# Performance work log

Hardware: AMD Instinct MI355X
Metric: run time of the kernel (lower is better)

The kernel has to match this reference:

```python
import jax, jax.numpy as jnp
import numpy as np

N = 10000      # nodes
E = 160000     # edges (before self-loops)
F_IN = 128     # num_features
H1, D1 = 4, 256   # conv1: 4 heads x 256, concat -> 1024
D2 = 256          # conv2: 1 head x 256
NEG_SLOPE = 0.2


def setup_inputs() -> dict:
    key = jax.random.key(0)
    ks = jax.random.split(key, 12)
    def p(k, shape, fan):
        return jax.random.normal(k, shape, jnp.float32) / np.float32(np.sqrt(fan))
    return {
        "x": jax.random.normal(ks[0], (N, F_IN), jnp.float32),
        "edge_index": jax.random.randint(ks[1], (2, E), 0, N, jnp.int32),
        "W1": p(ks[2], (F_IN, H1 * D1), F_IN),
        "att_src1": p(ks[3], (H1, D1), D1),
        "att_dst1": p(ks[4], (H1, D1), D1),
        "b1": jnp.zeros((H1 * D1,), jnp.float32),
        "lin1_W": p(ks[5], (F_IN, H1 * D1), F_IN),
        "lin1_b": jnp.zeros((H1 * D1,), jnp.float32),
        "W2": p(ks[6], (H1 * D1, D2), H1 * D1),
        "att_src2": p(ks[7], (1, D2), D2),
        "att_dst2": p(ks[8], (1, D2), D2),
        "b2": jnp.zeros((D2,), jnp.float32),
        "lin2_W": p(ks[9], (H1 * D1, D2), H1 * D1),
        "lin2_b": jnp.zeros((D2,), jnp.float32),
    }


def gat_layer(x, src, dst, W, a_src, a_dst, b, heads, d):
    """PyG-style GATConv: transform, edgewise LeakyReLU attention,
    segment-softmax over destination neighborhoods, scatter-add, concat heads."""
    n = x.shape[0]
    h = (x @ W).reshape(n, heads, d)                       # [N, H, D]
    s_src = jnp.einsum('nhd,hd->nh', h, a_src)             # per-node scores
    s_dst = jnp.einsum('nhd,hd->nh', h, a_dst)
    e = jax.nn.leaky_relu(s_src[src] + s_dst[dst], NEG_SLOPE)   # [E, H]
    m = jax.ops.segment_max(e, dst, num_segments=n)        # stable softmax per dst
    p = jnp.exp(e - m[dst])
    z = jax.ops.segment_sum(p, dst, num_segments=n)
    alpha = p / (z[dst] + 1e-16)                           # [E, H]
    msg = h[src] * alpha[:, :, None]                       # [E, H, D]
    out = jax.ops.segment_sum(msg, dst, num_segments=n)    # [N, H, D]
    return out.reshape(n, heads * d) + b, alpha


def reference(x, edge_index, W1, att_src1, att_dst1, b1, lin1_W, lin1_b,
              W2, att_src2, att_dst2, b2, lin2_W, lin2_b):
    n = x.shape[0]
    loop = jnp.arange(n, dtype=edge_index.dtype)           # add self-loops (PyG default)
    src = jnp.concatenate([edge_index[0], loop])
    dst = jnp.concatenate([edge_index[1], loop])
    h1, alpha1 = gat_layer(x, src, dst, W1, att_src1, att_dst1, b1, H1, D1)
    h1 = jax.nn.elu(h1 + x @ lin1_W + lin1_b)              # conv1 + lin1 residual, ELU
    h2, _ = gat_layer(h1, src, dst, W2, att_src2, att_dst2, b2, 1, D2)
    out = h2 + h1 @ lin2_W + lin2_b                        # conv2 + lin2 residual
    return out, alpha1
```

## Files before the change

### kernel.cpp

```cpp
#include <hip/hip_runtime.h>
#include <hip/hip_bf16.h>
#include <math.h>

#define NN   10000
#define EE   160000
#define ETOT 170000
#define FIN  128
#define C1   1024
#define NH1  4
#define D1   256
#define D2   256

typedef __attribute__((ext_vector_type(8))) short bf16x8;
typedef __attribute__((ext_vector_type(4))) float f32x4;

__device__ __forceinline__ float b2f(unsigned short u)
{
    union { unsigned int i; float f; } c; c.i = (unsigned int)u << 16; return c.f;
}
__device__ __forceinline__ unsigned short f2b(float x)
{
    return __builtin_bit_cast(unsigned short, __float2bfloat16(x));
}
__device__ __forceinline__ void split1(float x, unsigned short &h, unsigned short &l)
{
    __hip_bfloat16 hb = __float2bfloat16(x);
    float r = x - __bfloat162float(hb);
    h = __builtin_bit_cast(unsigned short, hb);
    l = __builtin_bit_cast(unsigned short, __float2bfloat16(r));
}

__global__ __launch_bounds__(256)
void split_A(const float* __restrict__ X, unsigned short* __restrict__ A2, int M, int K)
{
    int idx = blockIdx.x * 256 + threadIdx.x;
    int kq4 = K >> 2;
    if (idx >= M * kq4) return;
    int m = idx / kq4, kq = idx % kq4;
    float4 v = *(const float4*)&X[(size_t)m * K + kq * 4];
    ushort4 h, l;
    split1(v.x, h.x, l.x); split1(v.y, h.y, l.y);
    split1(v.z, h.z, l.z); split1(v.w, h.w, l.w);
    unsigned short* row = A2 + (size_t)m * (2 * K);
    *(ushort4*)&row[kq * 4]     = h;
    *(ushort4*)&row[K + kq * 4] = l;
}

__global__ __launch_bounds__(256)
void split_Bt(const float* __restrict__ B0, const float* __restrict__ B1,
              int K, int N0, int Ntot, unsigned short* __restrict__ Bt)
{
    int idx = blockIdx.x * 256 + threadIdx.x;
    int total = Ntot * (K >> 2);
    if (idx >= total) return;
    int n = idx % Ntot;
    int kq = idx / Ntot;
    int k = kq * 4;
    const float* B; int nc, nb;
    if (n < N0) { B = B0; nc = n; nb = N0; }
    else        { B = B1; nc = n - N0; nb = Ntot - N0; }
    float v0 = B[(size_t)(k + 0) * nb + nc];
    float v1 = B[(size_t)(k + 1) * nb + nc];
    float v2 = B[(size_t)(k + 2) * nb + nc];
    float v3 = B[(size_t)(k + 3) * nb + nc];
    ushort4 h, l;
    split1(v0, h.x, l.x); split1(v1, h.y, l.y);
    split1(v2, h.z, l.z); split1(v3, h.w, l.w);
    unsigned short* row = Bt + (size_t)n * (3 * K);
    *(ushort4*)&row[k]         = h;
    *(ushort4*)&row[K + k]     = h;
    *(ushort4*)&row[2 * K + k] = l;
}

__device__ __forceinline__ void glds16(const void* g, void* l)
{
    __builtin_amdgcn_global_load_lds((const __attribute__((address_space(1))) void*)g,
                                     (__attribute__((address_space(3))) void*)l, 16, 0, 0);
}

template<int BN, int WM, int WN>
__global__ __launch_bounds__(256)
void gemm_split(const unsigned short* __restrict__ A, int lda, int ka2,
                const unsigned short* __restrict__ Bt, int keff,
                unsigned short* __restrict__ outPb, float* __restrict__ outR,
                int M, int nsplit, int ldR,
                const float* __restrict__ bias0, const float* __restrict__ bias1)
{
    constexpr int BM  = 128;
    constexpr int WTM = BM / WM;
    constexpr int WTN = BN / WN;
    constexpr int FJ  = WTM / 16;
    constexpr int FI  = WTN / 16;
    constexpr int NCH = (BM + BN) / 16;
    constexpr int CPW = NCH / 4;

    __shared__ __align__(16) unsigned short sA[BM * 32];
    __shared__ __align__(16) unsigned short sB[BN * 32];
    const int tid = threadIdx.x;
    const int w = tid >> 6, lane = tid & 63;
    const int m0 = blockIdx.y * BM;
    const int n0 = blockIdx.x * BN;
    const int wm = w / WN, wn = w % WN;

    f32x4 acc[FI][FJ] = {};

    const unsigned short* gp[CPW];
    unsigned short*       lp[CPW];
    bool isa[CPW];
    #pragma unroll
    for (int cc = 0; cc < CPW; ++cc) {
        int c = w * CPW + cc;
        if (c < BM / 16) {
            int gm = m0 + c * 16 + (lane >> 2);
            if (gm >= M) gm = M - 1;
            gp[cc] = A + (size_t)gm * lda + (lane & 3) * 8;
            lp[cc] = &sA[c * 512];
            isa[cc] = true;
        } else {
            int r = (c - BM / 16) * 16 + (lane >> 2);
            gp[cc] = Bt + (size_t)(n0 + r) * keff + (lane & 3) * 8;
            lp[cc] = &sB[(c - BM / 16) * 512];
            isa[cc] = false;
        }
    }

    const int rA = wm * WTM + (lane & 15);
    const int rB = wn * WTN + (lane & 15);
    const int koff = (lane >> 4) * 8;

    for (int kk = 0; kk < keff; kk += 32) {
        const int kA = (kk >= ka2) ? (kk - ka2) : kk;
        #pragma unroll
        for (int cc = 0; cc < CPW; ++cc)
            glds16(gp[cc] + (isa[cc] ? kA : kk), lp[cc]);
        __syncthreads();
        bf16x8 av[FJ], bv[FI];
        #pragma unroll
        for (int f = 0; f < FI; ++f)
            bv[f] = *(const bf16x8*)&sB[(rB + f * 16) * 32 + koff];
        #pragma unroll
        for (int f = 0; f < FJ; ++f)
            av[f] = *(const bf16x8*)&sA[(rA + f * 16) * 32 + koff];
        #pragma unroll
        for (int fj = 0; fj < FJ; ++fj)
            #pragma unroll
            for (int fi = 0; fi < FI; ++fi)
                acc[fi][fj] = __builtin_amdgcn_mfma_f32_16x16x32_bf16(
                    bv[fi], av[fj], acc[fi][fj], 0, 0, 0);
        __syncthreads();
    }

    const int lrow = lane & 15;
    const int lcol = (lane >> 4) << 2;
    #pragma unroll
    for (int fj = 0; fj < FJ; ++fj) {
        int row = m0 + wm * WTM + fj * 16 + lrow;
        if (row >= M) continue;
        #pragma unroll
        for (int fi = 0; fi < FI; ++fi) {
            int col = n0 + wn * WTN + fi * 16 + lcol;
            f32x4 v = acc[fi][fj];
            if (col < nsplit) {
                ushort4 o;
                o.x = f2b(v[0]); o.y = f2b(v[1]); o.z = f2b(v[2]); o.w = f2b(v[3]);
                *(ushort4*)&outPb[(size_t)row * nsplit + col] = o;
            } else {
                int c = col - nsplit;
                const float4 g0 = *(const float4*)&bias0[c];
                const float4 g1 = *(const float4*)&bias1[c];
                v[0] += g0.x + g1.x; v[1] += g0.y + g1.y;
                v[2] += g0.z + g1.z; v[3] += g0.w + g1.w;
                *(f32x4*)&outR[(size_t)row * ldR + c] = v;
            }
        }
    }
}

__global__ __launch_bounds__(256)
void scores_h4(const unsigned short* __restrict__ h, const float* __restrict__ a_src,
               const float* __restrict__ a_dst, float* __restrict__ s_src,
               float* __restrict__ s_dst)
{
    const int n = blockIdx.x;
    const int w = threadIdx.x >> 6;
    const int lane = threadIdx.x & 63;
    ushort4 u = *(const ushort4*)&h[(size_t)n * C1 + w * D1 + lane * 4];
    float4 as = ((const float4*)&a_src[w * D1])[lane];
    float4 ad = ((const float4*)&a_dst[w * D1])[lane];
    float vx = b2f(u.x), vy = b2f(u.y), vz = b2f(u.z), vw = b2f(u.w);
    float ss = vx * as.x + vy * as.y + vz * as.z + vw * as.w;
    float sd = vx * ad.x + vy * ad.y + vz * ad.z + vw * ad.w;
    #pragma unroll
    for (int off = 32; off; off >>= 1) {
        ss += __shfl_xor(ss, off);
        sd += __shfl_xor(sd, off);
    }
    if (lane == 0) { s_src[n * NH1 + w] = ss; s_dst[n * NH1 + w] = sd; }
}

__global__ __launch_bounds__(256)
void scores_h1(const unsigned short* __restrict__ h, const float* __restrict__ a_src,
               const float* __restrict__ a_dst, float* __restrict__ s_src,
               float* __restrict__ s_dst)
{
    const int n = blockIdx.x * 4 + (threadIdx.x >> 6);
    if (n >= NN) return;
    const int lane = threadIdx.x & 63;
    ushort4 u = *(const ushort4*)&h[(size_t)n * D2 + lane * 4];
    float4 as = ((const float4*)a_src)[lane];
    float4 ad = ((const float4*)a_dst)[lane];
    float vx = b2f(u.x), vy = b2f(u.y), vz = b2f(u.z), vw = b2f(u.w);
    float ss = vx * as.x + vy * as.y + vz * as.z + vw * as.w;
    float sd = vx * ad.x + vy * ad.y + vz * ad.z + vw * ad.w;
    #pragma unroll
    for (int off = 32; off; off >>= 1) {
        ss += __shfl_xor(ss, off);
        sd += __shfl_xor(sd, off);
    }
    if (lane == 0) { s_src[n] = ss; s_dst[n] = sd; }
}

__global__ void count_deg(const int* __restrict__ dstp, int* __restrict__ cnt)
{
    int e = blockIdx.x * 256 + threadIdx.x;
    if (e >= ETOT) return;
    int d = (e < EE) ? dstp[e] : (e - EE);
    atomicAdd(&cnt[d], 1);
}

__global__ __launch_bounds__(1024)
void scan_kernel(const int* __restrict__ cnt, int* __restrict__ row_ptr)
{
    __shared__ int part[1024];
    const int t = threadIdx.x;
    int local[10];
    int s = 0;
    #pragma unroll
    for (int j = 0; j < 10; ++j) {
        int idx = t * 10 + j;
        local[j] = s;
        s += (idx < NN) ? cnt[idx] : 0;
    }
    part[t] = s;
    __syncthreads();
    for (int off = 1; off < 1024; off <<= 1) {
        int v = (t >= off) ? part[t - off] : 0;
        __syncthreads();
        part[t] += v;
        __syncthreads();
    }
    int prefix = (t > 0) ? part[t - 1] : 0;
    #pragma unroll
    for (int j = 0; j < 10; ++j) {
        int idx = t * 10 + j;
        if (idx < NN) row_ptr[idx] = prefix + local[j];
    }
    if (t == 0) row_ptr[NN] = ETOT;
}

__global__ void scatter_edges(const int* __restrict__ srcp, const int* __restrict__ dstp,
                              const int* __restrict__ row_ptr, int* __restrict__ fill,
                              int* __restrict__ csr_src, int* __restrict__ csr_eid)
{
    int e = blockIdx.x * 256 + threadIdx.x;
    if (e >= ETOT) return;
    int s, d;
    if (e < EE) { s = srcp[e]; d = dstp[e]; } else { s = d = e - EE; }
    int pos = row_ptr[d] + atomicAdd(&fill[d], 1);
    csr_src[pos] = s;
    csr_eid[pos] = e;
}

__global__ __launch_bounds__(256)
void aggregate1(const unsigned short* __restrict__ h1b, const float* __restrict__ s_src,
                const float* __restrict__ s_dst,
                const int* __restrict__ row_ptr, const int* __restrict__ csr_src,
                const int* __restrict__ csr_eid, const float* __restrict__ base_in,
                unsigned short* __restrict__ a2stk, float* __restrict__ alpha_out)
{
    const int n = blockIdx.x;
    const int t = threadIdx.x;
    const int h = t >> 6;
    const int lane = t & 63;
    const int start = row_ptr[n], end = row_ptr[n + 1];
    const float sd = s_dst[n * NH1 + h];

    float m = -1e30f;
    for (int i = start + lane; i < end; i += 64) {
        float sc = s_src[csr_src[i] * NH1 + h] + sd;
        sc = sc > 0.f ? sc : 0.2f * sc;
        m = fmaxf(m, sc);
    }
    #pragma unroll
    for (int off = 32; off; off >>= 1) m = fmaxf(m, __shfl_xor(m, off));
    float z = 0.f;
    for (int i = start + lane; i < end; i += 64) {
        float sc = s_src[csr_src[i] * NH1 + h] + sd;
        sc = sc > 0.f ? sc : 0.2f * sc;
        z += __expf(sc - m);
    }
    #pragma unroll
    for (int off = 32; off; off >>= 1) z += __shfl_xor(z, off);
    const float invz = 1.f / (z + 1e-16f);
    for (int i = start + lane; i < end; i += 64) {
        float sc = s_src[csr_src[i] * NH1 + h] + sd;
        sc = sc > 0.f ? sc : 0.2f * sc;
        alpha_out[(size_t)csr_eid[i] * NH1 + h] = __expf(sc - m) * invz;
    }

    float4 base = *(const float4*)&base_in[(size_t)n * C1 + t * 4];
    float4 acc = make_float4(0.f, 0.f, 0.f, 0.f);
    for (int i = start; i < end; ++i) {
        const int s = csr_src[i];
        float sc = s_src[s * NH1 + h] + sd;
        sc = sc > 0.f ? sc : 0.2f * sc;
        const float a = __expf(sc - m) * invz;
        ushort4 v = *(const ushort4*)&h1b[(size_t)s * C1 + t * 4];
        acc.x += a * b2f(v.x); acc.y += a * b2f(v.y);
        acc.z += a * b2f(v.z); acc.w += a * b2f(v.w);
    }
    float4 r;
    r.x = acc.x + base.x; r.y = acc.y + base.y;
    r.z = acc.z + base.z; r.w = acc.w + base.w;
    r.x = r.x > 0.f ? r.x : expm1f(r.x);
    r.y = r.y > 0.f ? r.y : expm1f(r.y);
    r.z = r.z > 0.f ? r.z : expm1f(r.z);
    r.w = r.w > 0.f ? r.w : expm1f(r.w);
    __syncthreads();
    ushort4 hi, lo;
    split1(r.x, hi.x, lo.x); split1(r.y, hi.y, lo.y);
    split1(r.z, hi.z, lo.z); split1(r.w, hi.w, lo.w);
    unsigned short* row = a2stk + (size_t)n * (2 * C1);
    *(ushort4*)&row[t * 4]      = hi;
    *(ushort4*)&row[C1 + t * 4] = lo;
}

__global__ __launch_bounds__(64)
void aggregate2(const unsigned short* __restrict__ h2b, const float* __restrict__ s_src,
                const float* __restrict__ s_dst,
                const int* __restrict__ row_ptr, const int* __restrict__ csr_src,
                const float* __restrict__ accin, float* __restrict__ out)
{
    const int n = blockIdx.x;
    const int t = threadIdx.x;
    const int start = row_ptr[n], end = row_ptr[n + 1];
    const float sd = s_dst[n];

    float m = -1e30f;
    for (int i = start + t; i < end; i += 64) {
        float sc = s_src[csr_src[i]] + sd;
        sc = sc > 0.f ? sc : 0.2f * sc;
        m = fmaxf(m, sc);
    }
    #pragma unroll
    for (int off = 32; off; off >>= 1) m = fmaxf(m, __shfl_xor(m, off));
    float z = 0.f;
    for (int i = start + t; i < end; i += 64) {
        float sc = s_src[csr_src[i]] + sd;
        sc = sc > 0.f ? sc : 0.2f * sc;
        z += __expf(sc - m);
    }
    #pragma unroll
    for (int off = 32; off; off >>= 1) z += __shfl_xor(z, off);
    const float invz = 1.f / (z + 1e-16f);

    float4 acc = make_float4(0.f, 0.f, 0.f, 0.f);
    for (int i = start; i < end; ++i) {
        const int s = csr_src[i];
        float sc = s_src[s] + sd;
        sc = sc > 0.f ? sc : 0.2f * sc;
        const float a = __expf(sc - m) * invz;
        ushort4 v = *(const ushort4*)&h2b[(size_t)s * D2 + t * 4];
        acc.x += a * b2f(v.x); acc.y += a * b2f(v.y);
        acc.z += a * b2f(v.z); acc.w += a * b2f(v.w);
    }
    float4 base = *(const float4*)&accin[(size_t)n * D2 + t * 4];
    float4 r;
    r.x = acc.x + base.x; r.y = acc.y + base.y;
    r.z = acc.z + base.z; r.w = acc.w + base.w;
    *(float4*)&out[(size_t)n * D2 + t * 4] = r;
}

extern "C" void kernel_launch(void* const* d_in, const int* in_sizes, int n_in,
                              void* d_out, int out_size, void* d_ws, size_t ws_size,
                              hipStream_t stream)
{
    const float* x        = (const float*)d_in[0];
    const int*   ei       = (const int*)  d_in[1];
    const float* W1       = (const float*)d_in[2];
    const float* att_src1 = (const float*)d_in[3];
    const float* att_dst1 = (const float*)d_in[4];
    const float* b1       = (const float*)d_in[5];
    const float* lin1_W   = (const float*)d_in[6];
    const float* lin1_b   = (const float*)d_in[7];
    const float* W2       = (const float*)d_in[8];
    const float* att_src2 = (const float*)d_in[9];
    const float* att_dst2 = (const float*)d_in[10];
    const float* b2       = (const float*)d_in[11];
    const float* lin2_W   = (const float*)d_in[12];
    const float* lin2_b   = (const float*)d_in[13];
    const int* srcp = ei;
    const int* dstp = ei + EE;

    float* out    = (float*)d_out;
    float* alpha1 = out + (size_t)NN * D2;

    float* fw = (float*)d_ws;
    float* acc1   = fw;   fw += (size_t)NN * C1;
    unsigned short* h1b = (unsigned short*)fw; fw += (size_t)NN * C1 / 2;
    unsigned short* h2b = (unsigned short*)fw; fw += (size_t)NN * D2 / 2;
    float* acc2   = fw;   fw += (size_t)NN * D2;
    unsigned short* A1stk = (unsigned short*)fw; fw += (size_t)NN * FIN;
    unsigned short* Bt1   = (unsigned short*)fw; fw += (size_t)2048 * 3 * FIN / 2;
    unsigned short* Bt2   = (unsigned short*)fw; fw += (size_t)512 * 3 * C1 / 2;
    float* s_src1 = fw;   fw += NN * NH1;
    float* s_dst1 = fw;   fw += NN * NH1;
    float* s_src2 = fw;   fw += NN;
    float* s_dst2 = fw;   fw += NN;
    int* ip      = (int*)fw;
    int* cnt     = ip;    ip += NN;
    int* fill    = ip;    ip += NN;
    int* row_ptr = ip;    ip += NN + 4;
    int* csr_src = ip;    ip += ETOT;
    int* csr_eid = ip;    ip += ETOT;

    unsigned short* A2stk = (unsigned short*)acc1;

    hipMemsetAsync(cnt, 0, 2 * NN * sizeof(int), stream);

    const int mt = (NN + 127) / 128;

    split_A<<<(NN * (FIN / 4) + 255) / 256, 256, 0, stream>>>(x, A1stk, NN, FIN);
    split_Bt<<<(2048 * (FIN / 4) + 255) / 256, 256, 0, stream>>>(W1, lin1_W, FIN, C1, 2048, Bt1);
    gemm_split<128, 2, 2><<<dim3(16, mt), 256, 0, stream>>>(
        A1stk, 2 * FIN, 2 * FIN, Bt1, 3 * FIN, h1b, acc1, NN, C1, C1, lin1_b, b1);
    scores_h4<<<NN, 256, 0, stream>>>(h1b, att_src1, att_dst1, s_src1, s_dst1);

    count_deg<<<(ETOT + 255) / 256, 256, 0, stream>>>(dstp, cnt);
    scan_kernel<<<1, 1024, 0, stream>>>(cnt, row_ptr);
    scatter_edges<<<(ETOT + 255) / 256, 256, 0, stream>>>(srcp, dstp, row_ptr, fill,
                                                          csr_src, csr_eid);

    aggregate1<<<NN, 256, 0, stream>>>(h1b, s_src1, s_dst1, row_ptr, csr_src, csr_eid,
                                       acc1, A2stk, alpha1);

    split_Bt<<<(512 * (C1 / 4) + 255) / 256, 256, 0, stream>>>(W2, lin2_W, C1, D2, 512, Bt2);
    gemm_split<64, 4, 1><<<dim3(8, mt), 256, 0, stream>>>(
        A2stk, 2 * C1, 2 * C1, Bt2, 3 * C1, h2b, acc2, NN, D2, D2, lin2_b, b2);

    scores_h1<<<(NN + 3) / 4, 256, 0, stream>>>(h2b, att_src2, att_dst2, s_src2, s_dst2);
    aggregate2<<<NN, 64, 0, stream>>>(h2b, s_src2, s_dst2, row_ptr, csr_src, acc2, out);
}
```

Before: 268.8 us.

## Double-buffer GEMM LDS tiles with XOR swizzle and XCD-aware tile remap

```diff
diff --git a/kernel.cpp b/kernel.cpp
--- a/kernel.cpp
+++ b/kernel.cpp
@@ -78,76 +78,112 @@
                                      (__attribute__((address_space(3))) void*)l, 16, 0, 0);
 }
 
-template<int BN, int WM, int WN>
+template<int BN, int WM, int WN, int BK>
 __global__ __launch_bounds__(256)
 void gemm_split(const unsigned short* __restrict__ A, int lda, int ka2,
                 const unsigned short* __restrict__ Bt, int keff,
                 unsigned short* __restrict__ outPb, float* __restrict__ outR,
-                int M, int nsplit, int ldR,
+                int M, int nsplit, int ldR, int ntn,
                 const float* __restrict__ bias0, const float* __restrict__ bias1)
 {
-    constexpr int BM  = 128;
-    constexpr int WTM = BM / WM;
-    constexpr int WTN = BN / WN;
-    constexpr int FJ  = WTM / 16;
-    constexpr int FI  = WTN / 16;
-    constexpr int NCH = (BM + BN) / 16;
-    constexpr int CPW = NCH / 4;
-
-    __shared__ __align__(16) unsigned short sA[BM * 32];
-    __shared__ __align__(16) unsigned short sB[BN * 32];
+    constexpr int BM   = 128;
+    constexpr int WTM  = BM / WM,  WTN = BN / WN;
+    constexpr int FJ   = WTM / 16, FI  = WTN / 16;
+    constexpr int KS   = BK / 32;
+    constexpr int SLOTS = BK / 8;
+    constexpr int SMASK = SLOTS - 1;
+    constexpr int SWSH  = (BK == 32) ? 1 : 0;
+    constexpr int RPC  = 512 / BK;
+    constexpr int ACH  = BM / RPC;
+    constexpr int NCH  = (BM + BN) / RPC;
+    constexpr int CPW  = NCH / 4;
+    constexpr int ABUF = BM * BK, BBUF = BN * BK;
+
+    __shared__ __align__(16) unsigned short sA[2 * ABUF];
+    __shared__ __align__(16) unsigned short sB[2 * BBUF];
+
     const int tid = threadIdx.x;
     const int w = tid >> 6, lane = tid & 63;
-    const int m0 = blockIdx.y * BM;
-    const int n0 = blockIdx.x * BN;
+
+    const int cpx = gridDim.x >> 3;
+    const int t0  = (blockIdx.x & 7) * cpx + (blockIdx.x >> 3);
+    const int m0 = (t0 / ntn) * BM;
+    const int n0 = (t0 % ntn) * BN;
     const int wm = w / WN, wn = w % WN;
 
     f32x4 acc[FI][FJ] = {};
 
     const unsigned short* gp[CPW];
-    unsigned short*       lp[CPW];
+    int lofs[CPW];
     bool isa[CPW];
-    #pragma unroll
-    for (int cc = 0; cc < CPW; ++cc) {
-        int c = w * CPW + cc;
-        if (c < BM / 16) {
-            int gm = m0 + c * 16 + (lane >> 2);
-            if (gm >= M) gm = M - 1;
-            gp[cc] = A + (size_t)gm * lda + (lane & 3) * 8;
-            lp[cc] = &sA[c * 512];
-            isa[cc] = true;
-        } else {
-            int r = (c - BM / 16) * 16 + (lane >> 2);
-            gp[cc] = Bt + (size_t)(n0 + r) * keff + (lane & 3) * 8;
-            lp[cc] = &sB[(c - BM / 16) * 512];
-            isa[cc] = false;
+    {
+        const int r  = lane / SLOTS;
+        const int sl = lane % SLOTS;
+        const int ssl = sl ^ ((r >> SWSH) & SMASK);
+        #pragma unroll
+        for (int cc = 0; cc < CPW; ++cc) {
+            int c = w * CPW + cc;
+            if (c < ACH) {
+                int gm = m0 + c * RPC + r; if (gm >= M) gm = M - 1;
+                gp[cc]   = A + (size_t)gm * lda + ssl * 8;
+                lofs[cc] = c * 512;
+                isa[cc]  = true;
+            } else {
+                int gn = n0 + (c - ACH) * RPC + r;
+                gp[cc]   = Bt + (size_t)gn * keff + ssl * 8;
+                lofs[cc] = (c - ACH) * 512;
+                isa[cc]  = false;
+            }
         }
     }
 
-    const int rA = wm * WTM + (lane & 15);
-    const int rB = wn * WTN + (lane & 15);
+    const int rAl = wm * WTM + (lane & 15);
+    const int rBl = wn * WTN + (lane & 15);
     const int koff = (lane >> 4) * 8;
-
-    for (int kk = 0; kk < keff; kk += 32) {
-        const int kA = (kk >= ka2) ? (kk - ka2) : kk;
+    const int nit = keff / BK;
+    int cur = 0;
+
+    #pragma unroll
+    for (int cc = 0; cc < CPW; ++cc)
+        glds16(gp[cc], (isa[cc] ? sA : sB) + lofs[cc]);
+    __syncthreads();
+
+    for (int it = 0; it < nit; ++it) {
+        if (it + 1 < nit) {
+            int kn = (it + 1) * BK;
+            int kAn = (kn >= ka2) ? (kn - ka2) : kn;
+            #pragma unroll
+            for (int cc = 0; cc < CPW; ++cc) {
+                unsigned short* dst = (isa[cc] ? sA + (cur ^ 1) * ABUF
+                                               : sB + (cur ^ 1) * BBUF) + lofs[cc];
+                glds16(gp[cc] + (isa[cc] ? kAn : kn), dst);
+            }
+        }
+        const unsigned short* cA = sA + cur * ABUF;
+        const unsigned short* cB = sB + cur * BBUF;
         #pragma unroll
-        for (int cc = 0; cc < CPW; ++cc)
-            glds16(gp[cc] + (isa[cc] ? kA : kk), lp[cc]);
+        for (int ks = 0; ks < KS; ++ks) {
+            const int sIdx = (ks * 32 + koff) >> 3;
+            bf16x8 av[FJ], bv[FI];
+            #pragma unroll
+            for (int f = 0; f < FI; ++f) {
+                int row = rBl + f * 16;
+                bv[f] = *(const bf16x8*)&cB[row * BK + ((sIdx ^ ((row >> SWSH) & SMASK)) << 3)];
+            }
+            #pragma unroll
+            for (int f = 0; f < FJ; ++f) {
+                int row = rAl + f * 16;
+                av[f] = *(const bf16x8*)&cA[row * BK + ((sIdx ^ ((row >> SWSH) & SMASK)) << 3)];
+            }
+            #pragma unroll
+            for (int fj = 0; fj < FJ; ++fj)
+                #pragma unroll
+                for (int fi = 0; fi < FI; ++fi)
+                    acc[fi][fj] = __builtin_amdgcn_mfma_f32_16x16x32_bf16(
+                        bv[fi], av[fj], acc[fi][fj], 0, 0, 0);
+        }
         __syncthreads();
-        bf16x8 av[FJ], bv[FI];
-        #pragma unroll
-        for (int f = 0; f < FI; ++f)
-            bv[f] = *(const bf16x8*)&sB[(rB + f * 16) * 32 + koff];
-        #pragma unroll
-        for (int f = 0; f < FJ; ++f)
-            av[f] = *(const bf16x8*)&sA[(rA + f * 16) * 32 + koff];
-        #pragma unroll
-        for (int fj = 0; fj < FJ; ++fj)
-            #pragma unroll
-            for (int fi = 0; fi < FI; ++fi)
-                acc[fi][fj] = __builtin_amdgcn_mfma_f32_16x16x32_bf16(
-                    bv[fi], av[fj], acc[fi][fj], 0, 0, 0);
-        __syncthreads();
+        cur ^= 1;
     }
 
     const int lrow = lane & 15;
@@ -432,8 +468,8 @@
 
     split_A<<<(NN * (FIN / 4) + 255) / 256, 256, 0, stream>>>(x, A1stk, NN, FIN);
     split_Bt<<<(2048 * (FIN / 4) + 255) / 256, 256, 0, stream>>>(W1, lin1_W, FIN, C1, 2048, Bt1);
-    gemm_split<128, 2, 2><<<dim3(16, mt), 256, 0, stream>>>(
-        A1stk, 2 * FIN, 2 * FIN, Bt1, 3 * FIN, h1b, acc1, NN, C1, C1, lin1_b, b1);
+    gemm_split<128, 2, 2, 32><<<mt * 16, 256, 0, stream>>>(
+        A1stk, 2 * FIN, 2 * FIN, Bt1, 3 * FIN, h1b, acc1, NN, C1, C1, 16, lin1_b, b1);
     scores_h4<<<NN, 256, 0, stream>>>(h1b, att_src1, att_dst1, s_src1, s_dst1);
 
     count_deg<<<(ETOT + 255) / 256, 256, 0, stream>>>(dstp, cnt);
@@ -445,8 +481,8 @@
                                        acc1, A2stk, alpha1);
 
     split_Bt<<<(512 * (C1 / 4) + 255) / 256, 256, 0, stream>>>(W2, lin2_W, C1, D2, 512, Bt2);
-    gemm_split<64, 4, 1><<<dim3(8, mt), 256, 0, stream>>>(
-        A2stk, 2 * C1, 2 * C1, Bt2, 3 * C1, h2b, acc2, NN, D2, D2, lin2_b, b2);
+    gemm_split<64, 4, 1, 64><<<mt * 8, 256, 0, stream>>>(
+        A2stk, 2 * C1, 2 * C1, Bt2, 3 * C1, h2b, acc2, NN, D2, D2, 8, lin2_b, b2);
 
     scores_h1<<<(NN + 3) / 4, 256, 0, stream>>>(h2b, att_src2, att_dst2, s_src2, s_dst2);
     aggregate2<<<NN, 64, 0, stream>>>(h2b, s_src2, s_dst2, row_ptr, csr_src, acc2, out);
```

Measured after the change: 236.3 us. -12.1%, faster.
